# Kernel tuning notes

Hardware: AMD Instinct MI355X
Metric: run time of the kernel (lower is better)

Reference implementation:

```python
import jax, jax.numpy as jnp
import numpy as np


def setup_inputs() -> dict:
    key = jax.random.key(0)
    n_clusters, dim_latent = 16, 64
    batch, L = 512, 10
    # upper-triangular pair indices (A, B) as in LatentSpace.__init__
    A_np, B_np = np.nonzero(np.triu(np.ones((n_clusters, n_clusters))))
    n_states = A_np.shape[0]  # 136
    k1, k2 = jax.random.split(key)
    z = jax.random.normal(k1, (batch, L, dim_latent), dtype=jnp.float32)
    mu = jax.random.uniform(k2, (dim_latent, n_clusters), dtype=jnp.float32,
                            minval=-1.0, maxval=1.0)
    pi = jnp.ones((1, n_states), jnp.float32) / n_states
    return {
        "z": z,
        "mu": mu,
        "pi": pi,
        "A": jnp.asarray(A_np, jnp.int32),
        "B": jnp.asarray(B_np, jnp.int32),
    }


def reference(z, mu, pi, A, B):
    """Faithful port of LatentSpace.call(z, inference=False) -> log_p_z (scalar)."""
    LOG2PI = jnp.log(jnp.asarray(2.0 * np.pi, jnp.float32))
    d = z.shape[-1]

    mu_A = mu[:, A]            # [d, S]
    mu_B = mu[:, B]            # [d, S]
    a1 = mu_B - mu_A           # [d, S]
    a2 = z[..., None] - mu_B[None, None]          # [b, L, d, S]

    inv_sig = jnp.sum(a1 * a1, axis=0)            # [S]
    # tf.math.reciprocal_no_nan: 0 where inv_sig == 0
    safe = jnp.where(inv_sig == 0, 1.0, inv_sig)
    recip = jnp.where(inv_sig == 0, 0.0, 1.0 / safe)

    _mu = -jnp.einsum('ds,blds->bls', a1, a2) * recip   # [b, L, S]
    sq_a2 = jnp.sum(a2 * a2, axis=2)                     # [b, L, S]
    _t = -sq_a2 + _mu ** 2 * inv_sig

    sd = jnp.sqrt(inv_sig + 1e-12)
    cdf = jax.scipy.special.ndtr  # gradient is the normal pdf, same as custom_gradient
    log_p_z_c_L = (0.5 * (LOG2PI - jnp.log(inv_sig + 1e-12) + _t)
                   + jnp.log(cdf((1.0 - _mu) * sd) - cdf(-_mu * sd) + 1e-12))

    log_pi = jnp.log(jax.nn.softmax(pi, axis=-1) + 1e-12)   # [1, S]
    log_p_zc_L = (-0.5 * d * LOG2PI
                  + log_pi[:, None, :]
                  + jnp.where(inv_sig == 0, -0.5 * sq_a2, log_p_z_c_L))  # [b, L, S]

    log_p_z_L = jax.scipy.special.logsumexp(log_p_zc_L, axis=-1, keepdims=True)
    log_p_z = jnp.mean(log_p_z_L)
    return log_p_z
```

## Files before the change

### kernel.cpp

```cpp
#include <hip/hip_runtime.h>
#include <math.h>

#define LOG2PI 1.8378770664093453f
#define NSTATES 136
#define NROWS 5120
#define DIM 64
#define NCLUST 16
#define NEG_BIG -1e30f

__device__ __forceinline__ float ndtrf(float x) {
    return 0.5f * erfcf(-x * 0.70710678118654752f);
}

__global__ __launch_bounds__(256) void state_consts_kernel(
    const float* __restrict__ mu,
    const float* __restrict__ pi,
    const int* __restrict__ A, const int* __restrict__ B,
    float4* __restrict__ k0, float4* __restrict__ k1,
    float* __restrict__ out)
{
    __shared__ float musm[DIM * NCLUST];
    __shared__ float pis[NSTATES];
    __shared__ float sm_m, sm_z;
    int tid = threadIdx.x;
    if (tid == 0) out[0] = 0.f;
    for (int i = tid; i < DIM * NCLUST; i += 256) musm[i] = mu[i];
    if (tid < NSTATES) pis[tid] = pi[tid];
    __syncthreads();
    if (tid < 64) {
        float m = NEG_BIG;
        for (int i = tid; i < NSTATES; i += 64) m = fmaxf(m, pis[i]);
        #pragma unroll
        for (int d = 1; d < 64; d <<= 1) m = fmaxf(m, __shfl_xor(m, d));
        float s = 0.f;
        for (int i = tid; i < NSTATES; i += 64) s += expf(pis[i] - m);
        #pragma unroll
        for (int d = 1; d < 64; d <<= 1) s += __shfl_xor(s, d);
        if (tid == 0) { sm_m = m; sm_z = s; }
    }
    __syncthreads();
    if (tid < NSTATES) {
        int a = A[tid], b = B[tid];
        float c1 = 0.f, nb2 = 0.f, iv = 0.f;
        for (int d = 0; d < DIM; ++d) {
            float mA = musm[d * NCLUST + a];
            float mB = musm[d * NCLUST + b];
            float a1 = mB - mA;
            c1  += a1 * mB;
            nb2 += mB * mB;
            iv  += a1 * a1;
        }
        float recip  = (iv == 0.f) ? 0.f : 1.f / iv;
        float sd     = sqrtf(iv + 1e-12f);
        float loginv = logf(iv + 1e-12f);
        float lp     = logf(expf(pis[tid] - sm_m) / sm_z + 1e-12f);
        float lcomb  = lp - 31.5f * LOG2PI - 0.5f * loginv;
        float lzero  = lp - 32.0f * LOG2PI;
        k0[tid] = make_float4(c1, nb2, recip, sd);
        k1[tid] = make_float4(lcomb, lzero, 0.f, 0.f);
    }
}

__global__ __launch_bounds__(256) void latent_main_kernel(
    const float* __restrict__ z,
    const float* __restrict__ mu,
    const int* __restrict__ A, const int* __restrict__ B,
    const float4* __restrict__ k0g, const float4* __restrict__ k1g,
    float* __restrict__ out)
{
    __shared__ float muT[NCLUST][68];
    __shared__ float4 k0s[NSTATES];
    __shared__ float4 k1s[NSTATES];
    __shared__ int2  abs_[NSTATES];
    __shared__ float redbuf[4];

    int tid = threadIdx.x;
    for (int i = tid; i < DIM * NCLUST; i += 256) {
        int d = i >> 4, c = i & 15;
        muT[c][d] = mu[i];
    }
    if (tid < NSTATES) {
        k0s[tid] = k0g[tid];
        k1s[tid] = k1g[tid];
        abs_[tid] = make_int2(A[tid], B[tid]);
    }
    __syncthreads();

    int w = tid >> 6, lane = tid & 63;
    int chunk = lane >> 4, c = lane & 15;
    int gw = blockIdx.x * 4 + w;

    float acc = 0.f;
    #pragma unroll
    for (int rr = 0; rr < 2; ++rr) {
        int r = gw * 2 + rr;

        const float4* zp = (const float4*)(z + (size_t)r * DIM + chunk * 16);
        const float4* mp = (const float4*)(&muT[c][chunk * 16]);
        float dotc = 0.f, zn = 0.f;
        #pragma unroll
        for (int i = 0; i < 4; ++i) {
            float4 z4 = zp[i];
            float4 m4 = mp[i];
            dotc += z4.x * m4.x + z4.y * m4.y + z4.z * m4.z + z4.w * m4.w;
            zn   += z4.x * z4.x + z4.y * z4.y + z4.z * z4.z + z4.w * z4.w;
        }
        dotc += __shfl_xor(dotc, 16);
        dotc += __shfl_xor(dotc, 32);
        zn   += __shfl_xor(zn, 16);
        zn   += __shfl_xor(zn, 32);

        float vals[3];
        #pragma unroll
        for (int it = 0; it < 3; ++it) {
            int s = it * 64 + lane;
            bool valid = (s < NSTATES);
            int ss = valid ? s : 0;
            int2 ab = abs_[ss];
            float4 K0 = k0s[ss];
            float4 K1 = k1s[ss];
            float cza = __shfl(dotc, ab.x);
            float czb = __shfl(dotc, ab.y);
            float dot = czb - cza - K0.x;
            float sq  = zn - 2.f * czb + K0.y;
            float mu_ = -dot * K0.z;
            float t   = -sq + dot * dot * K0.z;
            float dcdf = ndtrf((1.f - mu_) * K0.w) - ndtrf(-mu_ * K0.w);
            float v_n = K1.x + 0.5f * t + logf(dcdf + 1e-12f);
            float v_z = K1.y - 0.5f * sq;
            float v = (K0.z == 0.f) ? v_z : v_n;
            vals[it] = valid ? v : NEG_BIG;
        }

        float m = fmaxf(fmaxf(vals[0], vals[1]), vals[2]);
        float s = expf(vals[0] - m) + expf(vals[1] - m) + expf(vals[2] - m);
        #pragma unroll
        for (int d = 1; d < 64; d <<= 1) {
            float mo = __shfl_xor(m, d);
            float so = __shfl_xor(s, d);
            float mn = fmaxf(m, mo);
            s = s * expf(m - mn) + so * expf(mo - mn);
            m = mn;
        }
        acc += m + logf(s);
    }

    if (lane == 0) redbuf[w] = acc;
    __syncthreads();
    if (tid == 0) {
        float t = redbuf[0] + redbuf[1] + redbuf[2] + redbuf[3];
        atomicAdd(out, t * (1.0f / (float)NROWS));
    }
}

extern "C" void kernel_launch(void* const* d_in, const int* in_sizes, int n_in,
                              void* d_out, int out_size, void* d_ws, size_t ws_size,
                              hipStream_t stream) {
    const float* z  = (const float*)d_in[0];
    const float* mu = (const float*)d_in[1];
    const float* pi = (const float*)d_in[2];
    const int*   A  = (const int*)d_in[3];
    const int*   B  = (const int*)d_in[4];
    float* out = (float*)d_out;

    float4* k0 = (float4*)d_ws;
    float4* k1 = k0 + NSTATES;

    state_consts_kernel<<<1, 256, 0, stream>>>(mu, pi, A, B, k0, k1, out);
    latent_main_kernel<<<640, 256, 0, stream>>>(z, mu, A, B, k0, k1, out);
}
```

Measured before the change: 79.25 us.

## Fuse per-state constant computation into main kernel and replace atomics with partial reduce

Every block now computes the 136 per-state constants (softmax of pi, pair dot products over mu) redundantly in shared memory instead of relying on a separate single-block prologue kernel. The final mean becomes a per-block partial write plus a small one-block reduction kernel instead of global atomicAdd. This removes the serial dependency on a tiny one-block kernel and contention on a single atomic. In exchange each block repeats the 64-iteration constant loop, and a second launch is still needed for the reduction.

```diff
diff --git a/kernel.cpp b/kernel.cpp
--- a/kernel.cpp
+++ b/kernel.cpp
@@ -6,83 +6,69 @@
 #define NROWS 5120
 #define DIM 64
 #define NCLUST 16
+#define NBLOCKS 640
 #define NEG_BIG -1e30f
 
 __device__ __forceinline__ float ndtrf(float x) {
     return 0.5f * erfcf(-x * 0.70710678118654752f);
 }
 
-__global__ __launch_bounds__(256) void state_consts_kernel(
+__global__ __launch_bounds__(256) void latent_fused_kernel(
+    const float* __restrict__ z,
     const float* __restrict__ mu,
     const float* __restrict__ pi,
     const int* __restrict__ A, const int* __restrict__ B,
-    float4* __restrict__ k0, float4* __restrict__ k1,
-    float* __restrict__ out)
+    float* __restrict__ partials)
 {
-    __shared__ float musm[DIM * NCLUST];
+    __shared__ float muT[NCLUST][68];
     __shared__ float pis[NSTATES];
+    __shared__ float4 k0s[NSTATES];
+    __shared__ float4 k1s[NSTATES];
+    __shared__ int2  abs_[NSTATES];
     __shared__ float sm_m, sm_z;
+    __shared__ float redbuf[4];
+
     int tid = threadIdx.x;
-    if (tid == 0) out[0] = 0.f;
-    for (int i = tid; i < DIM * NCLUST; i += 256) musm[i] = mu[i];
-    if (tid < NSTATES) pis[tid] = pi[tid];
+    for (int i = tid; i < DIM * NCLUST; i += 256) {
+        muT[i & 15][i >> 4] = mu[i];
+    }
+    if (tid < NSTATES) {
+        pis[tid] = pi[tid];
+        abs_[tid] = make_int2(A[tid], B[tid]);
+    }
     __syncthreads();
-    if (tid < 64) {
+
+    float c1 = 0.f, nb2 = 0.f, iv = 0.f;
+    if (tid >= 192) {
+        int l = tid - 192;
         float m = NEG_BIG;
-        for (int i = tid; i < NSTATES; i += 64) m = fmaxf(m, pis[i]);
+        for (int i = l; i < NSTATES; i += 64) m = fmaxf(m, pis[i]);
         #pragma unroll
         for (int d = 1; d < 64; d <<= 1) m = fmaxf(m, __shfl_xor(m, d));
         float s = 0.f;
-        for (int i = tid; i < NSTATES; i += 64) s += expf(pis[i] - m);
+        for (int i = l; i < NSTATES; i += 64) s += expf(pis[i] - m);
         #pragma unroll
         for (int d = 1; d < 64; d <<= 1) s += __shfl_xor(s, d);
-        if (tid == 0) { sm_m = m; sm_z = s; }
-    }
-    __syncthreads();
-    if (tid < NSTATES) {
-        int a = A[tid], b = B[tid];
-        float c1 = 0.f, nb2 = 0.f, iv = 0.f;
+        if (l == 0) { sm_m = m; sm_z = s; }
+    } else if (tid < NSTATES) {
+        int2 ab = abs_[tid];
         for (int d = 0; d < DIM; ++d) {
-            float mA = musm[d * NCLUST + a];
-            float mB = musm[d * NCLUST + b];
+            float mA = muT[ab.x][d];
+            float mB = muT[ab.y][d];
             float a1 = mB - mA;
             c1  += a1 * mB;
             nb2 += mB * mB;
             iv  += a1 * a1;
         }
+    }
+    __syncthreads();
+    if (tid < NSTATES) {
         float recip  = (iv == 0.f) ? 0.f : 1.f / iv;
         float sd     = sqrtf(iv + 1e-12f);
-        float loginv = logf(iv + 1e-12f);
         float lp     = logf(expf(pis[tid] - sm_m) / sm_z + 1e-12f);
-        float lcomb  = lp - 31.5f * LOG2PI - 0.5f * loginv;
-        float lzero  = lp - 32.0f * LOG2PI;
-        k0[tid] = make_float4(c1, nb2, recip, sd);
-        k1[tid] = make_float4(lcomb, lzero, 0.f, 0.f);
-    }
-}
-
-__global__ __launch_bounds__(256) void latent_main_kernel(
-    const float* __restrict__ z,
-    const float* __restrict__ mu,
-    const int* __restrict__ A, const int* __restrict__ B,
-    const float4* __restrict__ k0g, const float4* __restrict__ k1g,
-    float* __restrict__ out)
-{
-    __shared__ float muT[NCLUST][68];
-    __shared__ float4 k0s[NSTATES];
-    __shared__ float4 k1s[NSTATES];
-    __shared__ int2  abs_[NSTATES];
-    __shared__ float redbuf[4];
-
-    int tid = threadIdx.x;
-    for (int i = tid; i < DIM * NCLUST; i += 256) {
-        int d = i >> 4, c = i & 15;
-        muT[c][d] = mu[i];
-    }
-    if (tid < NSTATES) {
-        k0s[tid] = k0g[tid];
-        k1s[tid] = k1g[tid];
-        abs_[tid] = make_int2(A[tid], B[tid]);
+        k0s[tid] = make_float4(c1, nb2, recip, sd);
+        k1s[tid] = make_float4(lp - 31.5f * LOG2PI - 0.5f * logf(iv + 1e-12f),
+                               lp - 32.0f * LOG2PI, 0.f, 0.f);
     }
     __syncthreads();
 
@@ -148,9 +134,22 @@
     if (lane == 0) redbuf[w] = acc;
     __syncthreads();
     if (tid == 0) {
-        float t = redbuf[0] + redbuf[1] + redbuf[2] + redbuf[3];
-        atomicAdd(out, t * (1.0f / (float)NROWS));
+        partials[blockIdx.x] = redbuf[0] + redbuf[1] + redbuf[2] + redbuf[3];
     }
+}
+
+__global__ __launch_bounds__(256) void final_reduce_kernel(
+    const float* __restrict__ partials, float* __restrict__ out)
+{
+    __shared__ float rb[4];
+    int tid = threadIdx.x;
+    float s = 0.f;
+    for (int i = tid; i < NBLOCKS; i += 256) s += partials[i];
+    #pragma unroll
+    for (int d = 1; d < 64; d <<= 1) s += __shfl_xor(s, d);
+    if ((tid & 63) == 0) rb[tid >> 6] = s;
+    __syncthreads();
+    if (tid == 0) out[0] = (rb[0] + rb[1] + rb[2] + rb[3]) * (1.0f / (float)NROWS);
 }
 
 extern "C" void kernel_launch(void* const* d_in, const int* in_sizes, int n_in,
@@ -162,10 +161,8 @@
     const int*   A  = (const int*)d_in[3];
     const int*   B  = (const int*)d_in[4];
     float* out = (float*)d_out;
+    float* partials = (float*)d_ws;
 
-    float4* k0 = (float4*)d_ws;
-    float4* k1 = k0 + NSTATES;
-
-    state_consts_kernel<<<1, 256, 0, stream>>>(mu, pi, A, B, k0, k1, out);
-    latent_main_kernel<<<640, 256, 0, stream>>>(z, mu, A, B, k0, k1, out);
+    latent_fused_kernel<<<NBLOCKS, 256, 0, stream>>>(z, mu, pi, A, B, partials);
+    final_reduce_kernel<<<1, 256, 0, stream>>>(partials, out);
 }
```

Result: faster. 74.10 us (-6.5%).
